# Performance work log

Hardware: AMD Instinct MI355X
Metric: run time of the kernel (lower is better)

Reference implementation:

```python
import jax, jax.numpy as jnp
import numpy as np


def _scan_dir(x, Wih, Whh, b, reverse):
    # x: (B,T,D); Wih: (4H,D); Whh: (4H,H); b: (4H,)  (= b_ih+b_hh)
    B = x.shape[0]
    H = Whh.shape[1]
    xg = jnp.einsum('btd,gd->btg', x, Wih) + b          # (B,T,4H) precomputed input projections
    xg = jnp.swapaxes(xg, 0, 1)                          # (T,B,4H)

    def step(carry, g_t):
        h, c = carry
        g = g_t + h @ Whh.T
        i, f, gg, o = jnp.split(g, 4, axis=-1)           # PyTorch gate order: i,f,g,o
        c = jax.nn.sigmoid(f) * c + jax.nn.sigmoid(i) * jnp.tanh(gg)
        h = jax.nn.sigmoid(o) * jnp.tanh(c)
        return (h, c), h

    h0 = jnp.zeros((B, H), x.dtype)
    _, hs = jax.lax.scan(step, (h0, h0), xg, reverse=reverse)
    return jnp.swapaxes(hs, 0, 1)                        # (B,T,H), time order preserved


def _bilstm(x, Wih_f, Whh_f, b_f, Wih_b, Whh_b, b_b):
    out_f = _scan_dir(x, Wih_f, Whh_f, b_f, reverse=False)
    out_b = _scan_dir(x, Wih_b, Whh_b, b_b, reverse=True)
    return jnp.concatenate([out_f, out_b], axis=-1)      # (B,T,2H)


def setup_inputs() -> dict:
    key = jax.random.key(0)
    ks = iter(jax.random.split(key, 32))
    B, T = 1024, 128
    H1, H2 = 50, 150

    def p(shape, scale):
        return (jax.random.normal(next(ks), shape, dtype=jnp.float32) * scale)

    s1 = 1.0 / np.sqrt(H1)
    s2 = 1.0 / np.sqrt(H2)
    inp = {
        'x': jax.random.normal(next(ks), (B, 1, T), dtype=jnp.float32),
        'rrs': jax.random.normal(next(ks), (B, 4), dtype=jnp.float32),
        # layer 1: in_dim=1, H=50, bidirectional
        'l1_Wih_f': p((4 * H1, 1), s1), 'l1_Whh_f': p((4 * H1, H1), s1), 'l1_b_f': p((4 * H1,), s1),
        'l1_Wih_b': p((4 * H1, 1), s1), 'l1_Whh_b': p((4 * H1, H1), s1), 'l1_b_b': p((4 * H1,), s1),
        # layer 2: in_dim=100, H=150, bidirectional
        'l2_Wih_f': p((4 * H2, 2 * H1), s2), 'l2_Whh_f': p((4 * H2, H2), s2), 'l2_b_f': p((4 * H2,), s2),
        'l2_Wih_b': p((4 * H2, 2 * H1), s2), 'l2_Whh_b': p((4 * H2, H2), s2), 'l2_b_b': p((4 * H2,), s2),
        # heads
        'head_W': p((20, 2 * H2), 0.05), 'head_b': p((20,), 0.05),
        'pef1_W': p((10, 4), 0.05), 'pef1_b': p((10,), 0.05),
        'pef2_W': p((2, 10), 0.05), 'pef2_b': p((2,), 0.05),
        'fc_W': p((4, 30), 0.05), 'fc_b': p((4,), 0.05),
    }
    return inp


def reference(x, rrs,
              l1_Wih_f, l1_Whh_f, l1_b_f, l1_Wih_b, l1_Whh_b, l1_b_b,
              l2_Wih_f, l2_Whh_f, l2_b_f, l2_Wih_b, l2_Whh_b, l2_b_b,
              head_W, head_b, pef1_W, pef1_b, pef2_W, pef2_b, fc_W, fc_b):
    xt = jnp.transpose(x, (0, 2, 1))                     # (B,T,1)
    out1 = _bilstm(xt, l1_Wih_f, l1_Whh_f, l1_b_f, l1_Wih_b, l1_Whh_b, l1_b_b)   # (B,T,100)
    out2 = _bilstm(out1, l2_Wih_f, l2_Whh_f, l2_b_f, l2_Wih_b, l2_Whh_b, l2_b_b) # (B,T,300)
    net = out2[:, -1]                                    # (B,300)
    waveform_feat = jax.nn.leaky_relu(net @ head_W.T + head_b, 0.3)              # (B,20)
    pef = jax.nn.leaky_relu(rrs @ pef1_W.T + pef1_b, 0.3)                        # (B,10)
    pef_logits = pef @ pef2_W.T + pef2_b                                         # (B,2)
    feat = jnp.concatenate([waveform_feat, pef], axis=1)                         # (B,30)
    logits = feat @ fc_W.T + fc_b                                                # (B,4)
    return (waveform_feat, pef_logits, feat, logits)
```

## Files before the change

kernel.cpp:

```cpp
#include <hip/hip_runtime.h>


typedef unsigned short u16;
typedef unsigned int u32;
typedef float f32x4 __attribute__((ext_vector_type(4)));
typedef _Float16 f16x8 __attribute__((ext_vector_type(8)));
typedef short s16x8 __attribute__((ext_vector_type(8)));

#if __has_builtin(__builtin_amdgcn_mfma_f32_16x16x32_f16)
#define USE_F16 1
#else
#define USE_F16 0
#endif

#define B1 1024
#define TT 128

__device__ __forceinline__ u16 to_h(float x) {
#if USE_F16
    _Float16 h = (_Float16)x;
    return __builtin_bit_cast(u16, h);
#else
    u32 u = __builtin_bit_cast(u32, x);
    u32 r = u + 0x7FFFu + ((u >> 16) & 1u);
    return (u16)(r >> 16);
#endif
}
__device__ __forceinline__ float from_h(u16 s) {
#if USE_F16
    return (float)__builtin_bit_cast(_Float16, s);
#else
    u32 u = ((u32)s) << 16;
    return __builtin_bit_cast(float, u);
#endif
}

__device__ __forceinline__ f32x4 mfma16(uint4 a, uint4 b, f32x4 c) {
#if USE_F16
    return __builtin_amdgcn_mfma_f32_16x16x32_f16(
        __builtin_bit_cast(f16x8, a), __builtin_bit_cast(f16x8, b), c, 0, 0, 0);
#else
    return __builtin_amdgcn_mfma_f32_16x16x32_bf16(
        __builtin_bit_cast(s16x8, a), __builtin_bit_cast(s16x8, b), c, 0, 0, 0);
#endif
}

#define LOG2E 1.4426950408889634f
__device__ __forceinline__ float sigm(float x) {
    return __builtin_amdgcn_rcpf(1.f + __builtin_amdgcn_exp2f(-LOG2E * x));
}
__device__ __forceinline__ float tanh_(float x) {
    return 1.f - 2.f * __builtin_amdgcn_rcpf(1.f + __builtin_amdgcn_exp2f(2.f * LOG2E * x));
}

__device__ __forceinline__ void wg_barrier_lds() {
    __builtin_amdgcn_sched_barrier(0);
    asm volatile("s_waitcnt lgkmcnt(0)" ::: "memory");
    __builtin_amdgcn_s_barrier();
    __builtin_amdgcn_sched_barrier(0);
}

__device__ __forceinline__ void prep_frag_body(
    const float* __restrict__ Wih, const float* __restrict__ Whh,
    const float* __restrict__ bias, uint4* __restrict__ dst,
    int GR, int NW, int NP, int KT,
    int x_off, int x_len, int h_off, int h_len, int bias_k, int bid, int l)
{
    int tile = bid / KT, kt = bid - tile * KT;
    int ml = l & 15;
    int qq = ml >> 2, tau = ml & 3;
    int w = tile % NW, p = tile / NW;
    int jj = (w * 4 + qq) * NP + p;
    bool valid = jj < GR;
    int row = tau * GR + jj;
    u32 dw[4];
    #pragma unroll
    for (int d = 0; d < 4; ++d) {
        u16 hh[2];
        #pragma unroll
        for (int s = 0; s < 2; ++s) {
            int j = d * 2 + s;
            int k = kt * 32 + (l >> 4) * 8 + j;
            float val = 0.f;
            if (valid) {
                if (k >= x_off && k < x_off + x_len) val = Wih[row * x_len + (k - x_off)];
                else if (k >= h_off && k < h_off + h_len) val = Whh[row * h_len + (k - h_off)];
                else if (k == bias_k) val = bias[row];
            }
            hh[s] = to_h(val);
        }
        dw[d] = (u32)hh[0] | ((u32)hh[1] << 16);
    }
    uint4 o; o.x = dw[0]; o.y = dw[1]; o.z = dw[2]; o.w = dw[3];
    dst[bid * 64 + l] = o;
}

__global__ void prep_all(const float* __restrict__ W1ihF, const float* __restrict__ W1hhF,
                         const float* __restrict__ b1F,
                         const float* __restrict__ W1ihB, const float* __restrict__ W1hhB,
                         const float* __restrict__ b1B,
                         const float* __restrict__ W2ihF, const float* __restrict__ W2hhF,
                         const float* __restrict__ b2F, const float* __restrict__ W2ihB,
                         uint4* __restrict__ frag1f, uint4* __restrict__ frag1b,
                         uint4* __restrict__ frag2f, float* __restrict__ WtT)
{
    int bid = blockIdx.x;
    int l = threadIdx.x;
    if (bid < 32)
        prep_frag_body(W1ihF, W1hhF, b1F, frag1f, 50, 8, 2, 2, 0, 1, 1, 50, 63, bid, l);
    else if (bid < 64)
        prep_frag_body(W1ihB, W1hhB, b1B, frag1b, 50, 8, 2, 2, 0, 1, 1, 50, 63, bid - 32, l);
    else if (bid < 384)
        prep_frag_body(W2ihF, W2hhF, b2F, frag2f, 150, 8, 5, 8, 0, 100, 100, 150, 255, bid - 64, l);
    else {
        int idx = (bid - 384) * 64 + l;
        if (idx < 60000) {
            int k = idx / 600, g = idx - k * 600;
            WtT[idx] = W2ihB[g * 100 + k];
        }
    }
}

__global__ __launch_bounds__(512, 2) void l1_scan(
    const float* __restrict__ x, const uint4* __restrict__ fragF,
    const uint4* __restrict__ fragB, u16* __restrict__ out1f)
{
    const int tid = threadIdx.x;
    const int lane = tid & 63;
    const int w = tid >> 6;
    const int q = lane >> 4;
    const int b = lane & 15;
    const int blk = blockIdx.x;
    const int dir = blockIdx.y;
    const uint4* frag = dir ? fragB : fragF;

    __shared__ u16 v[2][1024];
    __shared__ float x_s[128][17];

    uint4 af[2][2];
    #pragma unroll
    for (int i = 0; i < 2; ++i)
        #pragma unroll
        for (int kt = 0; kt < 2; ++kt)
            af[i][kt] = frag[((w + 8 * i) * 2 + kt) * 64 + lane];

    const int b0 = blk * 16;
    for (int idx = tid; idx < 1024; idx += 512) ((u32*)v)[idx] = 0u;
    for (int idx = tid; idx < 2048; idx += 512) {
        int bb = idx >> 7, t = idx & 127;
        x_s[t][bb] = x[(size_t)(b0 + bb) * TT + t];
    }
    __syncthreads();
    const u16 oneh = to_h(1.0f);
    if (tid < 16) {
        v[0][(112 + tid) * 8 + 7] = oneh;
        v[1][(112 + tid) * 8 + 7] = oneh;
        v[0][tid * 8] = to_h(x[(size_t)(b0 + tid) * TT + (dir ? TT - 1 : 0)]);
    }
    const int jjb = (w * 4 + q) * 2;
    int vslot[2]; size_t eb[2];
    #pragma unroll
    for (int p = 0; p < 2; ++p) {
        int jj = jjb + p;
        int k = 1 + jj;
        vslot[p] = ((k >> 5) * 64 + ((k & 31) >> 3) * 16 + b) * 8 + (k & 7);
        int k2 = dir * 50 + jj;
        eb[p] = (((size_t)blk * 4 + (k2 >> 5)) * 64 + ((k2 & 31) >> 3) * 16 + b) * 8 + (k2 & 7);
    }
    float c[2] = {0.f, 0.f};
    __syncthreads();

#define L1_STEP(T, CUR) { \
    uint4 bf0 = *(const uint4*)&v[CUR][lane * 8]; \
    uint4 bf1 = *(const uint4*)&v[CUR][(64 + lane) * 8]; \
    f32x4 acc[2]; \
    _Pragma("unroll") for (int i = 0; i < 2; ++i) acc[i] = (f32x4){0.f, 0.f, 0.f, 0.f}; \
    _Pragma("unroll") for (int i = 0; i < 2; ++i) acc[i] = mfma16(af[i][0], bf0, acc[i]); \
    _Pragma("unroll") for (int i = 0; i < 2; ++i) acc[i] = mfma16(af[i][1], bf1, acc[i]); \
    const int tt = dir ? 127 - (T) : (T); \
    _Pragma("unroll") for (int p = 0; p < 2; ++p) { \
        if (jjb + p < 50) { \
            float ig = acc[p][0], fg = acc[p][1], gg = acc[p][2], og = acc[p][3]; \
            float cn = sigm(fg) * c[p] + sigm(ig) * tanh_(gg); \
            float hn = sigm(og) * tanh_(cn); \
            c[p] = cn; \
            u16 hb = to_h(hn); \
            out1f[eb[p] + (size_t)tt * 131072] = hb; \
            v[1 - (CUR)][vslot[p]] = hb; \
        } \
    } \
    if (tid < 16 && (T) < 127) \
        v[1 - (CUR)][tid * 8] = to_h(x_s[dir ? 126 - (T) : (T) + 1][tid]); \
    wg_barrier_lds(); }

    for (int t2 = 0; t2 < TT; t2 += 2) {
        L1_STEP(t2, 0)
        L1_STEP(t2 + 1, 1)
    }
#undef L1_STEP
}

__global__ __launch_bounds__(512, 2) void l2f_scan(
    const uint4* __restrict__ frag, const u16* __restrict__ out1f,
    float* __restrict__ net)
{
    const int tid = threadIdx.x;
    const int lane = tid & 63;
    const int w = tid >> 6;
    const int q = lane >> 4;
    const int b = lane & 15;
    const int blk = blockIdx.x;
    const int b0 = blk * 16;
    const uint4* o4 = (const uint4*)out1f;

    __shared__ u16 v[2][4096];

    uint4 af[5][8];
    #pragma unroll
    for (int i = 0; i < 5; ++i)
        #pragma unroll
        for (int kt = 0; kt < 8; ++kt)
            af[i][kt] = frag[((w + 8 * i) * 8 + kt) * 64 + lane];

    for (int idx = tid; idx < 4096; idx += 512) ((u32*)v)[idx] = 0u;

    uint4 pfA[4], pfB[4];
    #pragma unroll
    for (int ktx = 0; ktx < 4; ++ktx)
        pfA[ktx] = o4[((size_t)blk * 4 + ktx) * 64 + lane];

    __syncthreads();
    const u16 oneh = to_h(1.0f);
    if (tid < 16) {
        v[0][(496 + tid) * 8 + 7] = oneh;
        v[1][(496 + tid) * 8 + 7] = oneh;
    }

    const u32 umask = (q == 0) ? 0xFFFFFFFFu : 0u;
    const int jjb = (w * 4 + q) * 5;
    int vslot[5];
    #pragma unroll
    for (int p = 0; p < 5; ++p) {
        int k = 100 + jjb + p;
        vslot[p] = ((k >> 5) * 64 + ((k & 31) >> 3) * 16 + b) * 8 + (k & 7);
    }
    float c[5] = {0.f, 0.f, 0.f, 0.f, 0.f};
    __syncthreads();

#define L2F_STEP(T, CUR, PFC, PFN) { \
    const int tn = ((T) < 127) ? (T) + 1 : 127; \
    _Pragma("unroll") for (int ktx = 0; ktx < 4; ++ktx) \
        PFN[ktx] = o4[(((size_t)tn * 64 + blk) * 4 + ktx) * 64 + lane]; \
    uint4 bfu[5]; \
    _Pragma("unroll") for (int kh = 0; kh < 5; ++kh) \
        bfu[kh] = *(const uint4*)&v[CUR][((kh + 3) * 64 + lane) * 8]; \
    bfu[0].x |= PFC[3].x & umask; \
    bfu[0].y |= PFC[3].y & umask; \
    f32x4 acc[5]; \
    _Pragma("unroll") for (int i = 0; i < 5; ++i) acc[i] = (f32x4){0.f, 0.f, 0.f, 0.f}; \
    _Pragma("unroll") for (int kt = 0; kt < 3; ++kt) { \
        _Pragma("unroll") for (int i = 0; i < 5; ++i) \
            acc[i] = mfma16(af[i][kt], PFC[kt], acc[i]); } \
    _Pragma("unroll") for (int kh = 0; kh < 5; ++kh) { \
        _Pragma("unroll") for (int i = 0; i < 5; ++i) \
            acc[i] = mfma16(af[i][kh + 3], bfu[kh], acc[i]); } \
    _Pragma("unroll") for (int p = 0; p < 5; ++p) { \
        float ig = acc[p][0], fg = acc[p][1], gg = acc[p][2], og = acc[p][3]; \
        float cn = sigm(fg) * c[p] + sigm(ig) * tanh_(gg); \
        float hn = sigm(og) * tanh_(cn); \
        c[p] = cn; \
        if (jjb + p < 150) { \
            v[1 - (CUR)][vslot[p]] = to_h(hn); \
            if ((T) == 127) net[(size_t)(b0 + b) * 300 + jjb + p] = hn; \
        } \
    } \
    wg_barrier_lds(); }

    for (int t2 = 0; t2 < TT; t2 += 2) {
        L2F_STEP(t2, 0, pfA, pfB)
        L2F_STEP(t2 + 1, 1, pfB, pfA)
    }
#undef L2F_STEP
}

__global__ __launch_bounds__(640, 1) void l2b_step(
    const u16* __restrict__ out1f, const float* __restrict__ WtT,
    const float* __restrict__ bias, float* __restrict__ net)
{
    const int tid = threadIdx.x;
    const int blk = blockIdx.x;
    const int b0 = blk * 16;
    __shared__ alignas(16) float x_s[100][16];
    __shared__ alignas(16) float gbuf[16][644];
    for (int idx = tid; idx < 1600; idx += 640) {
        int k2 = idx >> 4, bb = idx & 15;
        x_s[k2][bb] = from_h(out1f[((((size_t)127 * 64 + blk) * 4 + (k2 >> 5)) * 64
                                    + ((k2 & 31) >> 3) * 16 + bb) * 8 + (k2 & 7)]);
    }
    __syncthreads();
    if (tid < 600) {
        int g = tid;
        float acc[16];
        #pragma unroll
        for (int bb = 0; bb < 16; ++bb) acc[bb] = 0.f;
        for (int k = 0; k < 100; ++k) {
            float wv = WtT[k * 600 + g];
            float4 xa = *(const float4*)&x_s[k][0];
            float4 xb = *(const float4*)&x_s[k][4];
            float4 xc = *(const float4*)&x_s[k][8];
            float4 xd = *(const float4*)&x_s[k][12];
            acc[0] = fmaf(wv, xa.x, acc[0]);  acc[1] = fmaf(wv, xa.y, acc[1]);
            acc[2] = fmaf(wv, xa.z, acc[2]);  acc[3] = fmaf(wv, xa.w, acc[3]);
            acc[4] = fmaf(wv, xb.x, acc[4]);  acc[5] = fmaf(wv, xb.y, acc[5]);
            acc[6] = fmaf(wv, xb.z, acc[6]);  acc[7] = fmaf(wv, xb.w, acc[7]);
            acc[8] = fmaf(wv, xc.x, acc[8]);  acc[9] = fmaf(wv, xc.y, acc[9]);
            acc[10] = fmaf(wv, xc.z, acc[10]); acc[11] = fmaf(wv, xc.w, acc[11]);
            acc[12] = fmaf(wv, xd.x, acc[12]); acc[13] = fmaf(wv, xd.y, acc[13]);
            acc[14] = fmaf(wv, xd.z, acc[14]); acc[15] = fmaf(wv, xd.w, acc[15]);
        }
        #pragma unroll
        for (int bb = 0; bb < 16; ++bb) gbuf[bb][g] = acc[bb];
    }
    __syncthreads();
    for (int idx = tid; idx < 2400; idx += 640) {
        int j = idx >> 4, bb = idx & 15;
        float ig = gbuf[bb][j]       + bias[j];
        float gg = gbuf[bb][j + 300] + bias[j + 300];
        float og = gbuf[bb][j + 450] + bias[j + 450];
        float cn = sigm(ig) * tanh_(gg);
        float hn = sigm(og) * tanh_(cn);
        net[(size_t)(b0 + bb) * 300 + 150 + j] = hn;
    }
}

__global__ void head1(const float* __restrict__ net, const float* __restrict__ rrs,
                      const float* __restrict__ headW, const float* __restrict__ headb,
                      const float* __restrict__ p1W, const float* __restrict__ p1b,
                      const float* __restrict__ p2W, const float* __restrict__ p2b,
                      float* __restrict__ out)
{
    int gid = blockIdx.x * 256 + threadIdx.x;
    int b = gid >> 2, og = gid & 3;
    float acc[5];
    #pragma unroll
    for (int o2 = 0; o2 < 5; ++o2) acc[o2] = headb[og * 5 + o2];
    const float* nb = net + (size_t)b * 300;
    for (int k = 0; k < 300; ++k) {
        float nv = nb[k];
        #pragma unroll
        for (int o2 = 0; o2 < 5; ++o2)
            acc[o2] = fmaf(headW[(og * 5 + o2) * 300 + k], nv, acc[o2]);
    }
    #pragma unroll
    for (int o2 = 0; o2 < 5; ++o2) {
        int o = og * 5 + o2;
        float vv = acc[o2] > 0.f ? acc[o2] : 0.3f * acc[o2];
        out[b * 20 + o] = vv;
        out[22528 + b * 30 + o] = vv;
    }
    if (og == 0) {
        float p[10];
        #pragma unroll
        for (int r = 0; r < 10; ++r) {
            float a = p1b[r];
            #pragma unroll
            for (int qq = 0; qq < 4; ++qq) a = fmaf(p1W[r * 4 + qq], rrs[b * 4 + qq], a);
            p[r] = a > 0.f ? a : 0.3f * a;
            out[22528 + b * 30 + 20 + r] = p[r];
        }
        #pragma unroll
        for (int s = 0; s < 2; ++s) {
            float a = p2b[s];
            #pragma unroll
            for (int r = 0; r < 10; ++r) a = fmaf(p2W[s * 10 + r], p[r], a);
            out[20480 + b * 2 + s] = a;
        }
    }
}

__global__ void head2(const float* __restrict__ fcW, const float* __restrict__ fcb,
                      float* __restrict__ out)
{
    int b = blockIdx.x * 256 + threadIdx.x;
    const float* feat = out + 22528 + b * 30;
    float f[30];
    #pragma unroll
    for (int k = 0; k < 30; ++k) f[k] = feat[k];
    #pragma unroll
    for (int s = 0; s < 4; ++s) {
        float a = fcb[s];
        #pragma unroll
        for (int k = 0; k < 30; ++k) a = fmaf(fcW[s * 30 + k], f[k], a);
        out[53248 + b * 4 + s] = a;
    }
}

extern "C" void kernel_launch(void* const* d_in, const int* in_sizes, int n_in,
                              void* d_out, int out_size, void* d_ws, size_t ws_size,
                              hipStream_t stream)
{
    const float* x     = (const float*)d_in[0];
    const float* rrs   = (const float*)d_in[1];
    const float* W1ihF = (const float*)d_in[2];
    const float* W1hhF = (const float*)d_in[3];
    const float* b1F   = (const float*)d_in[4];
    const float* W1ihB = (const float*)d_in[5];
    const float* W1hhB = (const float*)d_in[6];
    const float* b1B   = (const float*)d_in[7];
    const float* W2ihF = (const float*)d_in[8];
    const float* W2hhF = (const float*)d_in[9];
    const float* b2F   = (const float*)d_in[10];
    const float* W2ihB = (const float*)d_in[11];
    const float* b2B   = (const float*)d_in[13];
    const float* headW = (const float*)d_in[14];
    const float* headb = (const float*)d_in[15];
    const float* p1W   = (const float*)d_in[16];
    const float* p1b   = (const float*)d_in[17];
    const float* p2W   = (const float*)d_in[18];
    const float* p2b   = (const float*)d_in[19];
    const float* fcW   = (const float*)d_in[20];
    const float* fcb   = (const float*)d_in[21];
    float* out = (float*)d_out;

    char* ws = (char*)d_ws;
    uint4* frag1f = (uint4*)(ws + 0);
    uint4* frag1b = (uint4*)(ws + 32768);
    uint4* frag2f = (uint4*)(ws + 65536);
    float* WtT    = (float*)(ws + 393216);
    u16*   out1f  = (u16*)(ws + 655360);
    float* net    = (float*)(ws + 655360 + 33554432);
    (void)ws_size; (void)in_sizes; (void)n_in; (void)out_size;

    prep_all<<<1322, 64, 0, stream>>>(W1ihF, W1hhF, b1F, W1ihB, W1hhB, b1B,
                                      W2ihF, W2hhF, b2F, W2ihB,
                                      frag1f, frag1b, frag2f, WtT);
    l1_scan<<<dim3(64, 2), 512, 0, stream>>>(x, frag1f, frag1b, out1f);
    l2f_scan<<<64, 512, 0, stream>>>(frag2f, out1f, net);
    l2b_step<<<64, 640, 0, stream>>>(out1f, WtT, b2B, net);
    head1<<<16, 256, 0, stream>>>(net, rrs, headW, headb, p1W, p1b, p2W, p2b, out);
    head2<<<4, 256, 0, stream>>>(fcW, fcb, out);
}
```

Baseline: 295.4 us.

## Spread LSTM scan tiles over 12 waves and fuse gate math into one cell routine

Both recurrent scan kernels now launch 768 threads (12 waves) instead of 512, with gate-row tiles interleaved across waves. Each wave handles at most 4 tiles in layer 2 instead of 5, and fewer in layer 1, which shortens the per-step serial MFMA chain and the number of cells per lane. The gate nonlinearities are merged into a single lstm_cell that shares reciprocals across sigmoid/tanh using clamped exponentials. MFMA issue in layer 2 is wrapped in s_setprio, and the LDS operand loads are moved ahead of the global prefetch. More waves per block raises barrier cost per step and may cut occupancy; the algebraic reformulation changes rounding slightly.

```diff
diff --git a/kernel.cpp b/kernel.cpp
--- a/kernel.cpp
+++ b/kernel.cpp
@@ -52,6 +52,24 @@
 __device__ __forceinline__ float tanh_(float x) {
     return 1.f - 2.f * __builtin_amdgcn_rcpf(1.f + __builtin_amdgcn_exp2f(2.f * LOG2E * x));
 }
+__device__ __forceinline__ float clampf(float x, float k) {
+    return fminf(fmaxf(x, -k), k);
+}
+
+__device__ __forceinline__ float lstm_cell(float ig, float fg, float gg, float og,
+                                           float& c)
+{
+    float ei = __builtin_amdgcn_exp2f(-LOG2E * clampf(ig, 25.f));
+    float ef = __builtin_amdgcn_exp2f(-LOG2E * clampf(fg, 25.f));
+    float eg = __builtin_amdgcn_exp2f(2.f * LOG2E * clampf(gg, 15.f));
+    float P   = (1.f + ei) * (eg + 1.f);
+    float num = fmaf(c, P, (eg - 1.f) * (1.f + ef));
+    float cn  = num * __builtin_amdgcn_rcpf((1.f + ef) * P);
+    c = cn;
+    float eo = __builtin_amdgcn_exp2f(-LOG2E * clampf(og, 25.f));
+    float ec = __builtin_amdgcn_exp2f(2.f * LOG2E * clampf(cn, 15.f));
+    return (ec - 1.f) * __builtin_amdgcn_rcpf((1.f + eo) * (ec + 1.f));
+}
 
 __device__ __forceinline__ void wg_barrier_lds() {
     __builtin_amdgcn_sched_barrier(0);
@@ -63,14 +81,13 @@
 __device__ __forceinline__ void prep_frag_body(
     const float* __restrict__ Wih, const float* __restrict__ Whh,
     const float* __restrict__ bias, uint4* __restrict__ dst,
-    int GR, int NW, int NP, int KT,
-    int x_off, int x_len, int h_off, int h_len, int bias_k, int bid, int l)
+    int GR, int KT, int x_off, int x_len, int h_off, int h_len, int bias_k,
+    int bid, int l)
 {
     int tile = bid / KT, kt = bid - tile * KT;
     int ml = l & 15;
     int qq = ml >> 2, tau = ml & 3;
-    int w = tile % NW, p = tile / NW;
-    int jj = (w * 4 + qq) * NP + p;
+    int jj = tile * 4 + qq;
     bool valid = jj < GR;
     int row = tau * GR + jj;
     u32 dw[4];
@@ -107,11 +124,11 @@
     int bid = blockIdx.x;
     int l = threadIdx.x;
     if (bid < 32)
-        prep_frag_body(W1ihF, W1hhF, b1F, frag1f, 50, 8, 2, 2, 0, 1, 1, 50, 63, bid, l);
+        prep_frag_body(W1ihF, W1hhF, b1F, frag1f, 50, 2, 0, 1, 1, 50, 63, bid, l);
     else if (bid < 64)
-        prep_frag_body(W1ihB, W1hhB, b1B, frag1b, 50, 8, 2, 2, 0, 1, 1, 50, 63, bid - 32, l);
+        prep_frag_body(W1ihB, W1hhB, b1B, frag1b, 50, 2, 0, 1, 1, 50, 63, bid - 32, l);
     else if (bid < 384)
-        prep_frag_body(W2ihF, W2hhF, b2F, frag2f, 150, 8, 5, 8, 0, 100, 100, 150, 255, bid - 64, l);
+        prep_frag_body(W2ihF, W2hhF, b2F, frag2f, 150, 8, 0, 100, 100, 150, 255, bid - 64, l);
     else {
         int idx = (bid - 384) * 64 + l;
         if (idx < 60000) {
@@ -121,7 +138,7 @@
     }
 }
 
-__global__ __launch_bounds__(512, 2) void l1_scan(
+__global__ __launch_bounds__(768) void l1_scan(
     const float* __restrict__ x, const uint4* __restrict__ fragF,
     const uint4* __restrict__ fragB, u16* __restrict__ out1f)
 {
@@ -139,14 +156,17 @@
 
     uint4 af[2][2];
     #pragma unroll
-    for (int i = 0; i < 2; ++i)
-        #pragma unroll
-        for (int kt = 0; kt < 2; ++kt)
-            af[i][kt] = frag[((w + 8 * i) * 2 + kt) * 64 + lane];
+    for (int i = 0; i < 2; ++i) {
+        int tile = w + 12 * i;
+        if (tile <= 12)
+            #pragma unroll
+            for (int kt = 0; kt < 2; ++kt)
+                af[i][kt] = frag[(tile * 2 + kt) * 64 + lane];
+    }
 
     const int b0 = blk * 16;
-    for (int idx = tid; idx < 1024; idx += 512) ((u32*)v)[idx] = 0u;
-    for (int idx = tid; idx < 2048; idx += 512) {
+    for (int idx = tid; idx < 1024; idx += 768) ((u32*)v)[idx] = 0u;
+    for (int idx = tid; idx < 2048; idx += 768) {
         int bb = idx >> 7, t = idx & 127;
         x_s[t][bb] = x[(size_t)(b0 + bb) * TT + t];
     }
@@ -157,14 +177,13 @@
         v[1][(112 + tid) * 8 + 7] = oneh;
         v[0][tid * 8] = to_h(x[(size_t)(b0 + tid) * TT + (dir ? TT - 1 : 0)]);
     }
-    const int jjb = (w * 4 + q) * 2;
     int vslot[2]; size_t eb[2];
     #pragma unroll
     for (int p = 0; p < 2; ++p) {
-        int jj = jjb + p;
+        int jj = (w + 12 * p) * 4 + q;
         int k = 1 + jj;
         vslot[p] = ((k >> 5) * 64 + ((k & 31) >> 3) * 16 + b) * 8 + (k & 7);
-        int k2 = dir * 50 + jj;
+        int k2 = dir * 50 + (jj < 50 ? jj : 0);
         eb[p] = (((size_t)blk * 4 + (k2 >> 5)) * 64 + ((k2 & 31) >> 3) * 16 + b) * 8 + (k2 & 7);
     }
     float c[2] = {0.f, 0.f};
@@ -175,15 +194,17 @@
     uint4 bf1 = *(const uint4*)&v[CUR][(64 + lane) * 8]; \
     f32x4 acc[2]; \
     _Pragma("unroll") for (int i = 0; i < 2; ++i) acc[i] = (f32x4){0.f, 0.f, 0.f, 0.f}; \
-    _Pragma("unroll") for (int i = 0; i < 2; ++i) acc[i] = mfma16(af[i][0], bf0, acc[i]); \
-    _Pragma("unroll") for (int i = 0; i < 2; ++i) acc[i] = mfma16(af[i][1], bf1, acc[i]); \
+    _Pragma("unroll") for (int i = 0; i < 2; ++i) { \
+        if (w + 12 * i <= 12) { \
+            acc[i] = mfma16(af[i][0], bf0, acc[i]); \
+            acc[i] = mfma16(af[i][1], bf1, acc[i]); \
+        } \
+    } \
     const int tt = dir ? 127 - (T) : (T); \
     _Pragma("unroll") for (int p = 0; p < 2; ++p) { \
-        if (jjb + p < 50) { \
-            float ig = acc[p][0], fg = acc[p][1], gg = acc[p][2], og = acc[p][3]; \
-            float cn = sigm(fg) * c[p] + sigm(ig) * tanh_(gg); \
-            float hn = sigm(og) * tanh_(cn); \
-            c[p] = cn; \
+        int jj = (w + 12 * p) * 4 + q; \
+        if (jj < 50) { \
+            float hn = lstm_cell(acc[p][0], acc[p][1], acc[p][2], acc[p][3], c[p]); \
             u16 hb = to_h(hn); \
             out1f[eb[p] + (size_t)tt * 131072] = hb; \
             v[1 - (CUR)][vslot[p]] = hb; \
@@ -200,7 +221,7 @@
 #undef L1_STEP
 }
 
-__global__ __launch_bounds__(512, 2) void l2f_scan(
+__global__ __launch_bounds__(768) void l2f_scan(
     const uint4* __restrict__ frag, const u16* __restrict__ out1f,
     float* __restrict__ net)
 {
@@ -215,14 +236,17 @@
 
     __shared__ u16 v[2][4096];
 
-    uint4 af[5][8];
-    #pragma unroll
-    for (int i = 0; i < 5; ++i)
-        #pragma unroll
-        for (int kt = 0; kt < 8; ++kt)
-            af[i][kt] = frag[((w + 8 * i) * 8 + kt) * 64 + lane];
-
-    for (int idx = tid; idx < 4096; idx += 512) ((u32*)v)[idx] = 0u;
+    uint4 af[4][8];
+    #pragma unroll
+    for (int i = 0; i < 4; ++i) {
+        int tile = w + 12 * i;
+        if (tile <= 37)
+            #pragma unroll
+            for (int kt = 0; kt < 8; ++kt)
+                af[i][kt] = frag[(tile * 8 + kt) * 64 + lane];
+    }
+
+    for (int idx = tid; idx < 4096; idx += 768) ((u32*)v)[idx] = 0u;
 
     uint4 pfA[4], pfB[4];
     #pragma unroll
@@ -237,41 +261,47 @@
     }
 
     const u32 umask = (q == 0) ? 0xFFFFFFFFu : 0u;
-    const int jjb = (w * 4 + q) * 5;
-    int vslot[5];
-    #pragma unroll
-    for (int p = 0; p < 5; ++p) {
-        int k = 100 + jjb + p;
+    int vslot[4];
+    #pragma unroll
+    for (int p = 0; p < 4; ++p) {
+        int jj = (w + 12 * p) * 4 + q;
+        int k = 100 + (jj < 150 ? jj : 0);
         vslot[p] = ((k >> 5) * 64 + ((k & 31) >> 3) * 16 + b) * 8 + (k & 7);
     }
-    float c[5] = {0.f, 0.f, 0.f, 0.f, 0.f};
+    float c[4] = {0.f, 0.f, 0.f, 0.f};
     __syncthreads();
 
 #define L2F_STEP(T, CUR, PFC, PFN) { \
+    uint4 bfu[5]; \
+    _Pragma("unroll") for (int kh = 0; kh < 5; ++kh) \
+        bfu[kh] = *(const uint4*)&v[CUR][((kh + 3) * 64 + lane) * 8]; \
     const int tn = ((T) < 127) ? (T) + 1 : 127; \
     _Pragma("unroll") for (int ktx = 0; ktx < 4; ++ktx) \
         PFN[ktx] = o4[(((size_t)tn * 64 + blk) * 4 + ktx) * 64 + lane]; \
-    uint4 bfu[5]; \
-    _Pragma("unroll") for (int kh = 0; kh < 5; ++kh) \
-        bfu[kh] = *(const uint4*)&v[CUR][((kh + 3) * 64 + lane) * 8]; \
+    f32x4 acc[4]; \
+    _Pragma("unroll") for (int i = 0; i < 4; ++i) acc[i] = (f32x4){0.f, 0.f, 0.f, 0.f}; \
+    __builtin_amdgcn_s_setprio(1); \
+    _Pragma("unroll") for (int i = 0; i < 4; ++i) { \
+        if (w + 12 * i <= 37) { \
+            _Pragma("unroll") for (int kt = 0; kt < 3; ++kt) \
+                acc[i] = mfma16(af[i][kt], PFC[kt], acc[i]); \
+        } \
+    } \
     bfu[0].x |= PFC[3].x & umask; \
     bfu[0].y |= PFC[3].y & umask; \
-    f32x4 acc[5]; \
-    _Pragma("unroll") for (int i = 0; i < 5; ++i) acc[i] = (f32x4){0.f, 0.f, 0.f, 0.f}; \
-    _Pragma("unroll") for (int kt = 0; kt < 3; ++kt) { \
-        _Pragma("unroll") for (int i = 0; i < 5; ++i) \
-            acc[i] = mfma16(af[i][kt], PFC[kt], acc[i]); } \
-    _Pragma("unroll") for (int kh = 0; kh < 5; ++kh) { \
-        _Pragma("unroll") for (int i = 0; i < 5; ++i) \
-            acc[i] = mfma16(af[i][kh + 3], bfu[kh], acc[i]); } \
-    _Pragma("unroll") for (int p = 0; p < 5; ++p) { \
-        float ig = acc[p][0], fg = acc[p][1], gg = acc[p][2], og = acc[p][3]; \
-        float cn = sigm(fg) * c[p] + sigm(ig) * tanh_(gg); \
-        float hn = sigm(og) * tanh_(cn); \
-        c[p] = cn; \
-        if (jjb + p < 150) { \
+    _Pragma("unroll") for (int i = 0; i < 4; ++i) { \
+        if (w + 12 * i <= 37) { \
+            _Pragma("unroll") for (int kh = 0; kh < 5; ++kh) \
+                acc[i] = mfma16(af[i][kh + 3], bfu[kh], acc[i]); \
+        } \
+    } \
+    __builtin_amdgcn_s_setprio(0); \
+    _Pragma("unroll") for (int p = 0; p < 4; ++p) { \
+        int jj = (w + 12 * p) * 4 + q; \
+        if (jj < 150) { \
+            float hn = lstm_cell(acc[p][0], acc[p][1], acc[p][2], acc[p][3], c[p]); \
             v[1 - (CUR)][vslot[p]] = to_h(hn); \
-            if ((T) == 127) net[(size_t)(b0 + b) * 300 + jjb + p] = hn; \
+            if ((T) == 127) net[(size_t)(b0 + b) * 300 + jj] = hn; \
         } \
     } \
     wg_barrier_lds(); }
@@ -434,8 +464,8 @@
     prep_all<<<1322, 64, 0, stream>>>(W1ihF, W1hhF, b1F, W1ihB, W1hhB, b1B,
                                       W2ihF, W2hhF, b2F, W2ihB,
                                       frag1f, frag1b, frag2f, WtT);
-    l1_scan<<<dim3(64, 2), 512, 0, stream>>>(x, frag1f, frag1b, out1f);
-    l2f_scan<<<64, 512, 0, stream>>>(frag2f, out1f, net);
+    l1_scan<<<dim3(64, 2), 768, 0, stream>>>(x, frag1f, frag1b, out1f);
+    l2f_scan<<<64, 768, 0, stream>>>(frag2f, out1f, net);
     l2b_step<<<64, 640, 0, stream>>>(out1f, WtT, b2B, net);
     head1<<<16, 256, 0, stream>>>(net, rrs, headW, headb, p1W, p1b, p2W, p2b, out);
     head2<<<4, 256, 0, stream>>>(fcW, fcb, out);
```

Result: slower. 645.9 us (+118.6%).
